# Optimization experiments

Hardware: AMD Instinct MI355X
Metric: run time of the kernel (lower is better)

Reference implementation:

```python
import jax, jax.numpy as jnp
import numpy as np

IN_F, OUT_F, MAX_LEN = 768, 512, 1024
NEG_INF = -9e15

def leaky_relu(x, slope=0.2):
    return jnp.where(x >= 0, x, slope * x)

def setup_inputs() -> dict:
    key = jax.random.key(0)
    k1, k2, k3, k4, k5, k6, k7 = jax.random.split(key, 7)
    B, N = 8, 1024
    h = jax.random.normal(k1, (B, N, IN_F), dtype=jnp.float32)
    adj = jax.random.randint(k2, (B, N, N), 0, 2, dtype=jnp.int32)
    positions = jax.random.randint(k3, (B, N), 0, MAX_LEN, dtype=jnp.int64)
    # learned params (nn.Linear stores weight [out,in]; we keep [in,out] for x@W)
    W = jax.random.normal(k4, (IN_F, OUT_F), dtype=jnp.float32) / np.sqrt(IN_F)
    # a: Linear(2*OUT_F, 1) -> vector of length 2*OUT_F, split into a1 (self) / a2 (neighbor)
    a = jax.random.normal(k5, (2 * OUT_F,), dtype=jnp.float32) / np.sqrt(2 * OUT_F)
    pos_table = jax.random.normal(k6, (MAX_LEN, OUT_F), dtype=jnp.float32) * 0.02
    return {"h": h, "adj": adj, "positions": positions, "W": W, "a": a, "pos_table": pos_table}

def reference(h, adj, positions, W, a, pos_table):
    # Wh: [B,N,Do]
    Wh = jnp.einsum("bnd,do->bno", h, W) + pos_table[positions]
    # additive-attention trick: a([Wh_i ; Wh_j]) = Wh_i@a1 + Wh_j@a2
    a1, a2 = a[:OUT_F], a[OUT_F:]
    f1 = Wh @ a1  # [B,N] score contribution of source (repeat_interleave side)
    f2 = Wh @ a2  # [B,N] score contribution of target (repeat side)
    e = leaky_relu(f1[:, :, None] + f2[:, None, :])  # [B,N,N]
    e = jnp.where(adj > 0, e, NEG_INF)
    attention = jax.nn.softmax(e, axis=-1)  # [B,N,N]
    h_prime = jnp.einsum("bnm,bmo->bno", attention, Wh)  # [B,N,Do]
    return h_prime, attention
```

## Files before the change

### kernel.cpp

```cpp
#include <hip/hip_runtime.h>
#include <stdint.h>

#define BATCH 8
#define NNODE 1024
#define INF 768
#define OUTF 512
#define MTOT (BATCH * NNODE)

typedef __attribute__((ext_vector_type(8))) short short8;
typedef __attribute__((ext_vector_type(4))) short short4v;
typedef __attribute__((ext_vector_type(4))) float floatx4;

__device__ __forceinline__ unsigned short f2bf(float f) {
  union { float f; unsigned u; } v; v.f = f;
  unsigned r = v.u + 0x7fffu + ((v.u >> 16) & 1u);
  return (unsigned short)(r >> 16);
}

__device__ __forceinline__ void gload_lds16(const void* g, void* l) {
  __builtin_amdgcn_global_load_lds(
      (const __attribute__((address_space(1))) void*)g,
      (__attribute__((address_space(3))) void*)l, 16, 0, 0);
}

__global__ __launch_bounds__(256) void prep_kernel(
    const float* __restrict__ h, const float* __restrict__ W,
    short* __restrict__ hbf, short* __restrict__ Wt, float* __restrict__ f12) {
  __shared__ float tile[32][33];
  int bid = blockIdx.x;
  int t = threadIdx.x;
  if (bid < 3072) {
    size_t i = ((size_t)bid * 256 + t) * 8;
    float4 v0 = *(const float4*)&h[i];
    float4 v1 = *(const float4*)&h[i + 4];
    short8 o;
    o[0] = (short)f2bf(v0.x); o[1] = (short)f2bf(v0.y);
    o[2] = (short)f2bf(v0.z); o[3] = (short)f2bf(v0.w);
    o[4] = (short)f2bf(v1.x); o[5] = (short)f2bf(v1.y);
    o[6] = (short)f2bf(v1.z); o[7] = (short)f2bf(v1.w);
    *(short8*)&hbf[i] = o;
    if (bid < 16) {
      float4 z = make_float4(0.f, 0.f, 0.f, 0.f);
      *(float4*)&f12[bid * 1024 + t * 4] = z;
    }
  } else {
    int tb = bid - 3072;
    int o0 = (tb & 15) * 32;
    int k0 = (tb >> 4) * 32;
    int x = t & 31, y = t >> 5;
#pragma unroll
    for (int q = 0; q < 4; ++q) {
      int r = y * 4 + q;
      tile[r][x] = W[(size_t)(k0 + r) * OUTF + o0 + x];
    }
    __syncthreads();
#pragma unroll
    for (int q = 0; q < 4; ++q) {
      int r = y * 4 + q;
      Wt[(size_t)(o0 + r) * INF + k0 + x] = (short)f2bf(tile[x][r]);
    }
  }
}

__global__ __launch_bounds__(512) void gemm1_kernel(
    const short* __restrict__ hbf, const short* __restrict__ Wt,
    const int* __restrict__ positions, const float* __restrict__ pos_table,
    const float* __restrict__ a, float* __restrict__ f12,
    short* __restrict__ Wht) {
  __shared__ short smem[24576];
  int bid0 = blockIdx.x;
  int bid = (bid0 & 7) * 64 + (bid0 >> 3);
  int nt = bid & 3, mt = bid >> 2;
  int M0 = mt * 64, N0 = nt * 128;
  int t = threadIdx.x;
  int wv = t >> 6, lane = t & 63;
  int wr = (wv >> 2) * 32, wc = (wv & 3) * 32;
  int l16 = lane & 15, kq = lane >> 4;

  floatx4 acc[2][2] = {};

  auto stage = [&](int buf, int kt) {
    {
      int row = t >> 3;
      int cg = (t & 7) ^ (row & 7);
      gload_lds16(&hbf[(size_t)(M0 + row) * INF + kt * 64 + cg * 8],
                  &smem[buf * 4096 + (t >> 6) * 512 + (t & 63) * 8]);
    }
#pragma unroll
    for (int i = 0; i < 2; ++i) {
      int q = wv * 64 + lane + i * 512;
      int row = q >> 3;
      int cg = (q & 7) ^ (row & 7);
      gload_lds16(&Wt[(size_t)(N0 + row) * INF + kt * 64 + cg * 8],
                  &smem[8192 + buf * 8192 + (wv * 64 + i * 512) * 8]);
    }
  };

  stage(0, 0);
  __syncthreads();
  for (int kt = 0; kt < 12; ++kt) {
    if (kt < 11) stage((kt + 1) & 1, kt + 1);
    const short* As = &smem[(kt & 1) * 4096];
    const short* Bs = &smem[8192 + (kt & 1) * 8192];
#pragma unroll
    for (int ks = 0; ks < 2; ++ks) {
      short8 af[2], bfv[2];
#pragma unroll
      for (int mi = 0; mi < 2; ++mi) {
        int r = wr + mi * 16 + l16;
        af[mi] = *(const short8*)&As[r * 64 + (((ks * 4 + kq) ^ (r & 7)) * 8)];
      }
#pragma unroll
      for (int ni = 0; ni < 2; ++ni) {
        int r = wc + ni * 16 + l16;
        bfv[ni] = *(const short8*)&Bs[r * 64 + (((ks * 4 + kq) ^ (r & 7)) * 8)];
      }
#pragma unroll
      for (int mi = 0; mi < 2; ++mi)
#pragma unroll
        for (int ni = 0; ni < 2; ++ni)
          acc[mi][ni] = __builtin_amdgcn_mfma_f32_16x16x32_bf16(af[mi], bfv[ni], acc[mi][ni], 0, 0, 0);
    }
    __syncthreads();
  }

  int oc0 = N0 + wc + l16;
  int oc1 = oc0 + 16;
#pragma unroll
  for (int mi = 0; mi < 2; ++mi)
#pragma unroll
    for (int j = 0; j < 4; ++j) {
      int row = M0 + wr + mi * 16 + kq * 4 + j;
      int pos = positions[row];
      acc[mi][0][j] += pos_table[(size_t)pos * OUTF + oc0];
      acc[mi][1][j] += pos_table[(size_t)pos * OUTF + oc1];
    }
  short* T = smem;
#pragma unroll
  for (int mi = 0; mi < 2; ++mi)
#pragma unroll
    for (int ni = 0; ni < 2; ++ni)
#pragma unroll
      for (int j = 0; j < 4; ++j)
        T[(wc + ni * 16 + l16) * 72 + wr + mi * 16 + kq * 4 + j] =
            (short)f2bf(acc[mi][ni][j]);
  float a10 = a[oc0], a11 = a[oc1];
  float a20 = a[OUTF + oc0], a21 = a[OUTF + oc1];
  float v1[8], v2[8];
#pragma unroll
  for (int mi = 0; mi < 2; ++mi)
#pragma unroll
    for (int j = 0; j < 4; ++j) {
      v1[mi * 4 + j] = acc[mi][0][j] * a10 + acc[mi][1][j] * a11;
      v2[mi * 4 + j] = acc[mi][0][j] * a20 + acc[mi][1][j] * a21;
    }
#pragma unroll
  for (int mlen = 4; mlen >= 1; mlen >>= 1) {
    bool hi = (l16 & mlen) != 0;
#pragma unroll
    for (int i = 0; i < mlen; ++i) {
      float k1 = hi ? v1[mlen + i] : v1[i];
      float s1 = hi ? v1[i] : v1[mlen + i];
      float k2 = hi ? v2[mlen + i] : v2[i];
      float s2 = hi ? v2[i] : v2[mlen + i];
      v1[i] = k1 + __shfl_xor(s1, mlen);
      v2[i] = k2 + __shfl_xor(s2, mlen);
    }
  }
  v1[0] += __shfl_xor(v1[0], 8);
  v2[0] += __shfl_xor(v2[0], 8);
  if (l16 < 8) {
    int rrow = M0 + wr + ((l16 >> 2) & 1) * 16 + kq * 4 + (l16 & 3);
    atomicAdd(&f12[rrow], v1[0]);
    atomicAdd(&f12[MTOT + rrow], v2[0]);
  }
  __syncthreads();
  int bb = M0 >> 10, i0 = M0 & 1023;
#pragma unroll
  for (int i = 0; i < 2; ++i) {
    int c = t + i * 512;
    int row = c >> 3;
    int mc = (c & 7) * 8;
    short8 vv = *(const short8*)&T[row * 72 + mc];
    *(short8*)&Wht[((size_t)bb * OUTF + N0 + row) * NNODE + i0 + mc] = vv;
  }
}

__global__ __launch_bounds__(256) void softmax_kernel(
    const float* __restrict__ f1, const float* __restrict__ f2,
    const int* __restrict__ adj, float* __restrict__ att,
    short* __restrict__ attbf) {
  int m = blockIdx.x;
  int b = m >> 10;
  int t = threadIdx.x;
  int wave = t >> 6, lane = t & 63;
  __shared__ float red[4];
  float f1v = f1[m];
  int4 av = ((const int4*)(adj + (size_t)m * NNODE))[t];
  float4 fv = ((const float4*)(f2 + b * NNODE))[t];
  float e[4];
  {
    float x;
    x = f1v + fv.x; x = x >= 0.f ? x : 0.2f * x; e[0] = av.x > 0 ? x : -9e15f;
    x = f1v + fv.y; x = x >= 0.f ? x : 0.2f * x; e[1] = av.y > 0 ? x : -9e15f;
    x = f1v + fv.z; x = x >= 0.f ? x : 0.2f * x; e[2] = av.z > 0 ? x : -9e15f;
    x = f1v + fv.w; x = x >= 0.f ? x : 0.2f * x; e[3] = av.w > 0 ? x : -9e15f;
  }
  float mx = fmaxf(fmaxf(e[0], e[1]), fmaxf(e[2], e[3]));
#pragma unroll
  for (int off = 32; off; off >>= 1) mx = fmaxf(mx, __shfl_xor(mx, off));
  if (lane == 0) red[wave] = mx;
  __syncthreads();
  mx = fmaxf(fmaxf(red[0], red[1]), fmaxf(red[2], red[3]));
  __syncthreads();
  float p[4], s = 0.f;
#pragma unroll
  for (int q = 0; q < 4; ++q) { p[q] = expf(e[q] - mx); s += p[q]; }
#pragma unroll
  for (int off = 32; off; off >>= 1) s += __shfl_xor(s, off);
  if (lane == 0) red[wave] = s;
  __syncthreads();
  s = red[0] + red[1] + red[2] + red[3];
  float inv = 1.f / s;
  float4 o = make_float4(p[0] * inv, p[1] * inv, p[2] * inv, p[3] * inv);
  ((float4*)(att + (size_t)m * NNODE))[t] = o;
  short4v ob;
  ob[0] = (short)f2bf(o.x); ob[1] = (short)f2bf(o.y);
  ob[2] = (short)f2bf(o.z); ob[3] = (short)f2bf(o.w);
  ((short4v*)(attbf + (size_t)m * NNODE))[t] = ob;
}

__global__ __launch_bounds__(512) void pv_kernel(
    const short* __restrict__ attbf, const short* __restrict__ Wht,
    float* __restrict__ hp) {
  __shared__ short smem[24576];
  int bid0 = blockIdx.x;
  int bid = (bid0 & 7) * 64 + (bid0 >> 3);
  int nt = bid & 3, mt = bid >> 2;
  int M0 = mt * 64, N0 = nt * 128;
  const short* Wb = Wht + (size_t)(M0 >> 10) * OUTF * NNODE;
  int t = threadIdx.x;
  int wv = t >> 6, lane = t & 63;
  int wr = (wv >> 2) * 32, wc = (wv & 3) * 32;
  int l16 = lane & 15, kq = lane >> 4;

  floatx4 acc[2][2] = {};

  auto stage = [&](int buf, int kt) {
    {
      int row = t >> 3;
      int cg = (t & 7) ^ (row & 7);
      gload_lds16(&attbf[(size_t)(M0 + row) * NNODE + kt * 64 + cg * 8],
                  &smem[buf * 4096 + (t >> 6) * 512 + (t & 63) * 8]);
    }
#pragma unroll
    for (int i = 0; i < 2; ++i) {
      int q = wv * 64 + lane + i * 512;
      int row = q >> 3;
      int cg = (q & 7) ^ (row & 7);
      gload_lds16(&Wb[(size_t)(N0 + row) * NNODE + kt * 64 + cg * 8],
                  &smem[8192 + buf * 8192 + (wv * 64 + i * 512) * 8]);
    }
  };

  stage(0, 0);
  __syncthreads();
  for (int kt = 0; kt < 16; ++kt) {
    if (kt < 15) stage((kt + 1) & 1, kt + 1);
    const short* As = &smem[(kt & 1) * 4096];
    const short* Bs = &smem[8192 + (kt & 1) * 8192];
#pragma unroll
    for (int ks = 0; ks < 2; ++ks) {
      short8 af[2], bfv[2];
#pragma unroll
      for (int mi = 0; mi < 2; ++mi) {
        int r = wr + mi * 16 + l16;
        af[mi] = *(const short8*)&As[r * 64 + (((ks * 4 + kq) ^ (r & 7)) * 8)];
      }
#pragma unroll
      for (int ni = 0; ni < 2; ++ni) {
        int r = wc + ni * 16 + l16;
        bfv[ni] = *(const short8*)&Bs[r * 64 + (((ks * 4 + kq) ^ (r & 7)) * 8)];
      }
#pragma unroll
      for (int mi = 0; mi < 2; ++mi)
#pragma unroll
        for (int ni = 0; ni < 2; ++ni)
          acc[mi][ni] = __builtin_amdgcn_mfma_f32_16x16x32_bf16(af[mi], bfv[ni], acc[mi][ni], 0, 0, 0);
    }
    __syncthreads();
  }

#pragma unroll
  for (int mi = 0; mi < 2; ++mi)
#pragma unroll
    for (int j = 0; j < 4; ++j) {
      int row = M0 + wr + mi * 16 + kq * 4 + j;
#pragma unroll
      for (int ni = 0; ni < 2; ++ni) {
        int col = N0 + wc + ni * 16 + l16;
        hp[(size_t)row * OUTF + col] = acc[mi][ni][j];
      }
    }
}

extern "C" void kernel_launch(void* const* d_in, const int* in_sizes, int n_in,
                              void* d_out, int out_size, void* d_ws, size_t ws_size,
                              hipStream_t stream) {
  const float* h = (const float*)d_in[0];
  const int* adj = (const int*)d_in[1];
  const int* positions = (const int*)d_in[2];
  const float* W = (const float*)d_in[3];
  const float* a = (const float*)d_in[4];
  const float* pos_table = (const float*)d_in[5];

  float* hp = (float*)d_out;
  float* att = hp + (size_t)MTOT * OUTF;

  char* ws = (char*)d_ws;
  short* Wt = (short*)ws;
  short* Wht = (short*)(ws + 786432);
  float* f12 = (float*)(ws + 786432 + 8388608);
  short* hbf = (short*)(ws + 786432 + 8388608 + 65536);
  short* attbf = hbf;

  prep_kernel<<<3456, 256, 0, stream>>>(h, W, hbf, Wt, f12);
  gemm1_kernel<<<512, 512, 0, stream>>>(hbf, Wt, positions, pos_table, a, f12, Wht);
  softmax_kernel<<<8192, 256, 0, stream>>>(f12, f12 + MTOT, adj, att, attbf);
  pv_kernel<<<512, 512, 0, stream>>>(attbf, Wht, hp);
}
```

Baseline: 55.05 us.

## Load fp32 A operands directly into LDS and convert to bf16 at fragment load

The separate fp32-to-bf16 conversion pass over h in the prep kernel is removed, and so is the bf16 copy of the attention matrix written by softmax. Both GEMMs now stage the fp32 A tiles straight into LDS and convert them to bf16 with v_cvt_pk_bf16_f32 while building MFMA fragments. This cuts extra global write and read traffic and shrinks the prep kernel. In exchange, the A tile moves twice the bytes into LDS, LDS usage grows, and conversion work is repeated by each block that shares an A tile.

```diff
diff --git a/kernel.cpp b/kernel.cpp
--- a/kernel.cpp
+++ b/kernel.cpp
@@ -23,30 +23,24 @@
       (__attribute__((address_space(3))) void*)l, 16, 0, 0);
 }
 
+__device__ __forceinline__ short8 cvt8(float4 x0, float4 x1) {
+  union { unsigned u[4]; short8 s; } pk;
+  asm("v_cvt_pk_bf16_f32 %0, %1, %2" : "=v"(pk.u[0]) : "v"(x0.x), "v"(x0.y));
+  asm("v_cvt_pk_bf16_f32 %0, %1, %2" : "=v"(pk.u[1]) : "v"(x0.z), "v"(x0.w));
+  asm("v_cvt_pk_bf16_f32 %0, %1, %2" : "=v"(pk.u[2]) : "v"(x1.x), "v"(x1.y));
+  asm("v_cvt_pk_bf16_f32 %0, %1, %2" : "=v"(pk.u[3]) : "v"(x1.z), "v"(x1.w));
+  return pk.s;
+}
+
 __global__ __launch_bounds__(256) void prep_kernel(
-    const float* __restrict__ h, const float* __restrict__ W,
-    short* __restrict__ hbf, short* __restrict__ Wt, float* __restrict__ f12) {
+    const float* __restrict__ W, short* __restrict__ Wt,
+    float* __restrict__ f12) {
   __shared__ float tile[32][33];
   int bid = blockIdx.x;
   int t = threadIdx.x;
-  if (bid < 3072) {
-    size_t i = ((size_t)bid * 256 + t) * 8;
-    float4 v0 = *(const float4*)&h[i];
-    float4 v1 = *(const float4*)&h[i + 4];
-    short8 o;
-    o[0] = (short)f2bf(v0.x); o[1] = (short)f2bf(v0.y);
-    o[2] = (short)f2bf(v0.z); o[3] = (short)f2bf(v0.w);
-    o[4] = (short)f2bf(v1.x); o[5] = (short)f2bf(v1.y);
-    o[6] = (short)f2bf(v1.z); o[7] = (short)f2bf(v1.w);
-    *(short8*)&hbf[i] = o;
-    if (bid < 16) {
-      float4 z = make_float4(0.f, 0.f, 0.f, 0.f);
-      *(float4*)&f12[bid * 1024 + t * 4] = z;
-    }
-  } else {
-    int tb = bid - 3072;
-    int o0 = (tb & 15) * 32;
-    int k0 = (tb >> 4) * 32;
+  if (bid < 384) {
+    int o0 = (bid & 15) * 32;
+    int k0 = (bid >> 4) * 32;
     int x = t & 31, y = t >> 5;
 #pragma unroll
     for (int q = 0; q < 4; ++q) {
@@ -59,15 +53,20 @@
       int r = y * 4 + q;
       Wt[(size_t)(o0 + r) * INF + k0 + x] = (short)f2bf(tile[x][r]);
     }
+  } else {
+    int z = bid - 384;
+    float4 zz = make_float4(0.f, 0.f, 0.f, 0.f);
+    *(float4*)&f12[z * 1024 + t * 4] = zz;
   }
 }
 
 __global__ __launch_bounds__(512) void gemm1_kernel(
-    const short* __restrict__ hbf, const short* __restrict__ Wt,
+    const float* __restrict__ h, const short* __restrict__ Wt,
     const int* __restrict__ positions, const float* __restrict__ pos_table,
     const float* __restrict__ a, float* __restrict__ f12,
     short* __restrict__ Wht) {
-  __shared__ short smem[24576];
+  __shared__ float Af[2][4096];
+  __shared__ short Bsm[2][8192];
   int bid0 = blockIdx.x;
   int bid = (bid0 & 7) * 64 + (bid0 >> 3);
   int nt = bid & 3, mt = bid >> 2;
@@ -80,11 +79,13 @@
   floatx4 acc[2][2] = {};
 
   auto stage = [&](int buf, int kt) {
-    {
-      int row = t >> 3;
-      int cg = (t & 7) ^ (row & 7);
-      gload_lds16(&hbf[(size_t)(M0 + row) * INF + kt * 64 + cg * 8],
-                  &smem[buf * 4096 + (t >> 6) * 512 + (t & 63) * 8]);
+#pragma unroll
+    for (int i = 0; i < 2; ++i) {
+      int q = wv * 64 + lane + i * 512;
+      int row = q >> 4, c = q & 15;
+      int cg = c ^ ((row & 7) << 1);
+      gload_lds16(&h[(size_t)(M0 + row) * INF + kt * 64 + cg * 4],
+                  &Af[buf][(wv * 64 + i * 512) * 4]);
     }
 #pragma unroll
     for (int i = 0; i < 2; ++i) {
@@ -92,7 +93,7 @@
       int row = q >> 3;
       int cg = (q & 7) ^ (row & 7);
       gload_lds16(&Wt[(size_t)(N0 + row) * INF + kt * 64 + cg * 8],
-                  &smem[8192 + buf * 8192 + (wv * 64 + i * 512) * 8]);
+                  &Bsm[buf][(wv * 64 + i * 512) * 8]);
     }
   };
 
@@ -100,15 +101,17 @@
   __syncthreads();
   for (int kt = 0; kt < 12; ++kt) {
     if (kt < 11) stage((kt + 1) & 1, kt + 1);
-    const short* As = &smem[(kt & 1) * 4096];
-    const short* Bs = &smem[8192 + (kt & 1) * 8192];
+    const float* Ab = Af[kt & 1];
+    const short* Bs = Bsm[kt & 1];
 #pragma unroll
     for (int ks = 0; ks < 2; ++ks) {
       short8 af[2], bfv[2];
 #pragma unroll
       for (int mi = 0; mi < 2; ++mi) {
         int r = wr + mi * 16 + l16;
-        af[mi] = *(const short8*)&As[r * 64 + (((ks * 4 + kq) ^ (r & 7)) * 8)];
+        int c2 = ((ks * 4 + kq) * 2) ^ ((r & 7) << 1);
+        const float* src = &Ab[r * 64 + c2 * 4];
+        af[mi] = cvt8(*(const float4*)src, *(const float4*)(src + 4));
       }
 #pragma unroll
       for (int ni = 0; ni < 2; ++ni) {
@@ -135,7 +138,7 @@
       acc[mi][0][j] += pos_table[(size_t)pos * OUTF + oc0];
       acc[mi][1][j] += pos_table[(size_t)pos * OUTF + oc1];
     }
-  short* T = smem;
+  short* T = (short*)&Af[0][0];
 #pragma unroll
   for (int mi = 0; mi < 2; ++mi)
 #pragma unroll
@@ -188,8 +191,7 @@
 
 __global__ __launch_bounds__(256) void softmax_kernel(
     const float* __restrict__ f1, const float* __restrict__ f2,
-    const int* __restrict__ adj, float* __restrict__ att,
-    short* __restrict__ attbf) {
+    const int* __restrict__ adj, float* __restrict__ att) {
   int m = blockIdx.x;
   int b = m >> 10;
   int t = threadIdx.x;
@@ -224,16 +226,13 @@
   float inv = 1.f / s;
   float4 o = make_float4(p[0] * inv, p[1] * inv, p[2] * inv, p[3] * inv);
   ((float4*)(att + (size_t)m * NNODE))[t] = o;
-  short4v ob;
-  ob[0] = (short)f2bf(o.x); ob[1] = (short)f2bf(o.y);
-  ob[2] = (short)f2bf(o.z); ob[3] = (short)f2bf(o.w);
-  ((short4v*)(attbf + (size_t)m * NNODE))[t] = ob;
 }
 
 __global__ __launch_bounds__(512) void pv_kernel(
-    const short* __restrict__ attbf, const short* __restrict__ Wht,
+    const float* __restrict__ att, const short* __restrict__ Wht,
     float* __restrict__ hp) {
-  __shared__ short smem[24576];
+  __shared__ float Af[2][4096];
+  __shared__ short Bsm[2][8192];
   int bid0 = blockIdx.x;
   int bid = (bid0 & 7) * 64 + (bid0 >> 3);
   int nt = bid & 3, mt = bid >> 2;
@@ -247,11 +246,13 @@
   floatx4 acc[2][2] = {};
 
   auto stage = [&](int buf, int kt) {
-    {
-      int row = t >> 3;
-      int cg = (t & 7) ^ (row & 7);
-      gload_lds16(&attbf[(size_t)(M0 + row) * NNODE + kt * 64 + cg * 8],
-                  &smem[buf * 4096 + (t >> 6) * 512 + (t & 63) * 8]);
+#pragma unroll
+    for (int i = 0; i < 2; ++i) {
+      int q = wv * 64 + lane + i * 512;
+      int row = q >> 4, c = q & 15;
+      int cg = c ^ ((row & 7) << 1);
+      gload_lds16(&att[(size_t)(M0 + row) * NNODE + kt * 64 + cg * 4],
+                  &Af[buf][(wv * 64 + i * 512) * 4]);
     }
 #pragma unroll
     for (int i = 0; i < 2; ++i) {
@@ -259,7 +260,7 @@
       int row = q >> 3;
       int cg = (q & 7) ^ (row & 7);
       gload_lds16(&Wb[(size_t)(N0 + row) * NNODE + kt * 64 + cg * 8],
-                  &smem[8192 + buf * 8192 + (wv * 64 + i * 512) * 8]);
+                  &Bsm[buf][(wv * 64 + i * 512) * 8]);
     }
   };
 
@@ -267,15 +268,17 @@
   __syncthreads();
   for (int kt = 0; kt < 16; ++kt) {
     if (kt < 15) stage((kt + 1) & 1, kt + 1);
-    const short* As = &smem[(kt & 1) * 4096];
-    const short* Bs = &smem[8192 + (kt & 1) * 8192];
+    const float* Ab = Af[kt & 1];
+    const short* Bs = Bsm[kt & 1];
 #pragma unroll
     for (int ks = 0; ks < 2; ++ks) {
       short8 af[2], bfv[2];
 #pragma unroll
       for (int mi = 0; mi < 2; ++mi) {
         int r = wr + mi * 16 + l16;
-        af[mi] = *(const short8*)&As[r * 64 + (((ks * 4 + kq) ^ (r & 7)) * 8)];
+        int c2 = ((ks * 4 + kq) * 2) ^ ((r & 7) << 1);
+        const float* src = &Ab[r * 64 + c2 * 4];
+        af[mi] = cvt8(*(const float4*)src, *(const float4*)(src + 4));
       }
 #pragma unroll
       for (int ni = 0; ni < 2; ++ni) {
@@ -321,11 +324,9 @@
   short* Wt = (short*)ws;
   short* Wht = (short*)(ws + 786432);
   float* f12 = (float*)(ws + 786432 + 8388608);
-  short* hbf = (short*)(ws + 786432 + 8388608 + 65536);
-  short* attbf = hbf;
-
-  prep_kernel<<<3456, 256, 0, stream>>>(h, W, hbf, Wt, f12);
-  gemm1_kernel<<<512, 512, 0, stream>>>(hbf, Wt, positions, pos_table, a, f12, Wht);
-  softmax_kernel<<<8192, 256, 0, stream>>>(f12, f12 + MTOT, adj, att, attbf);
-  pv_kernel<<<512, 512, 0, stream>>>(attbf, Wht, hp);
-}
+
+  prep_kernel<<<400, 256, 0, stream>>>(W, Wt, f12);
+  gemm1_kernel<<<512, 512, 0, stream>>>(h, Wt, positions, pos_table, a, f12, Wht);
+  softmax_kernel<<<8192, 256, 0, stream>>>(f12, f12 + MTOT, adj, att);
+  pv_kernel<<<512, 512, 0, stream>>>(att, Wht, hp);
+}
```

After: 59.39 us. +7.9%, slower.
